# Kernel optimization log

Measured on AMD Instinct MI355X. Metric: run time of the kernel, lower is better.

Reference implementation:

```python
import jax, jax.numpy as jnp
import numpy as np

SIZE_MIN, SIZE_MAX = 10.0, 40.0
CROP = 28


def convert_to_box_list(x):
    # [B, C, W, H] -> [W*H, B, C]
    b, c, w, h = x.shape
    return jnp.transpose(x, (2, 3, 0, 1)).reshape(w * h, b, c)


def invert_convert_to_box_list(x, w, h):
    # [W*H, B, C] -> [B, C, W, H]
    n, b, c = x.shape
    return jnp.transpose(x.reshape(w, h, b, c), (2, 3, 0, 1))


def bilinear_sample(img, x, y):
    # img: [C, W, H]; x, y: pixel coords of shape S -> [C, *S]; zero outside.
    C, W, H = img.shape
    x0 = jnp.floor(x); y0 = jnp.floor(y)
    x1 = x0 + 1.0; y1 = y0 + 1.0
    wx1 = x - x0; wx0 = 1.0 - wx1
    wy1 = y - y0; wy0 = 1.0 - wy1
    def fetch(xi, yi):
        valid = ((xi >= 0) & (xi < W) & (yi >= 0) & (yi < H)).astype(img.dtype)
        xc = jnp.clip(xi, 0, W - 1).astype(jnp.int32)
        yc = jnp.clip(yi, 0, H - 1).astype(jnp.int32)
        return img[:, xc, yc] * valid
    return (fetch(x0, y0) * (wx0 * wy0) + fetch(x1, y0) * (wx1 * wy0)
            + fetch(x0, y1) * (wx0 * wy1) + fetch(x1, y1) * (wx1 * wy1))


def crop(bx, by, bw, bh, big, ws, hs):
    # bx..bh: [k, B]; big: [B, C, W, H] -> [k, B, C, ws, hs]
    u = (jnp.arange(ws) + 0.5) / ws
    v = (jnp.arange(hs) + 0.5) / hs
    xs = bx[..., None] - 0.5 * bw[..., None] + u * bw[..., None] - 0.5  # [k,B,ws]
    ys = by[..., None] - 0.5 * bh[..., None] + v * bh[..., None] - 0.5  # [k,B,hs]
    def one(xr, yr, img):
        X = jnp.broadcast_to(xr[:, None], (ws, hs))
        Y = jnp.broadcast_to(yr[None, :], (ws, hs))
        return bilinear_sample(img, X, Y)
    return jax.vmap(jax.vmap(one, (0, 0, 0)), (0, 0, None))(xs, ys, big)


def uncrop(bx, by, bw, bh, small, Wb, Hb):
    # small: [k, B, C, ws, hs] -> [k, B, C, Wb, Hb] (zero outside each box)
    ws, hs = small.shape[-2], small.shape[-1]
    Xc = jnp.arange(Wb) + 0.5
    Yc = jnp.arange(Hb) + 0.5
    xs = (Xc - (bx[..., None] - 0.5 * bw[..., None])) / bw[..., None] * ws - 0.5
    ys = (Yc - (by[..., None] - 0.5 * bh[..., None])) / bh[..., None] * hs - 0.5
    def one(xr, yr, img):
        X = jnp.broadcast_to(xr[:, None], (Wb, Hb))
        Y = jnp.broadcast_to(yr[None, :], (Wb, Hb))
        return bilinear_sample(img, X, Y)
    return jax.vmap(jax.vmap(one, (0, 0, 0)), (0, 0, 0))(xs, ys, small)


def tmaps_to_bb(tmaps, W_raw, H_raw):
    # tmaps: [B, 4, nw, nh] in (0,1) -> box lists [n_all, B]
    nw, nh = tmaps.shape[-2], tmaps.shape[-1]
    tx, ty, tw, th = tmaps[:, 0], tmaps[:, 1], tmaps[:, 2], tmaps[:, 3]
    ix = jnp.arange(nw, dtype=tmaps.dtype)[:, None]
    iy = jnp.arange(nh, dtype=tmaps.dtype)[None, :]
    bx_map = W_raw * (ix + tx) / nw
    by_map = H_raw * (iy + ty) / nh
    bw_map = SIZE_MIN + (SIZE_MAX - SIZE_MIN) * tw
    bh_map = SIZE_MIN + (SIZE_MAX - SIZE_MIN) * th
    tolist = lambda m: convert_to_box_list(m[:, None]).squeeze(-1)
    return tolist(bx_map), tolist(by_map), tolist(bw_map), tolist(bh_map)


def forward_core(logit_mu, zwhere_mu, zwhere_std, eps_zwhere, eps_zinstance,
                 features, w_zwhere, b_zwhere, w_enc, b_enc, w_dec, b_dec, n_objects_max):
    B, Cf, W_raw, H_raw = features.shape
    nw, nh = logit_mu.shape[-2], logit_mu.shape[-1]

    # zwhere posterior sample + KL vs N(0,1)
    zwhere_sample_map = zwhere_mu + zwhere_std * eps_zwhere
    zwhere_kl_map = 0.5 * (zwhere_mu ** 2 + zwhere_std ** 2) - jnp.log(zwhere_std) - 0.5

    # decode zwhere (1x1 conv) -> sigmoid tmaps -> boxes
    tmaps = jax.nn.sigmoid(jnp.einsum('bzwh,cz->bcwh', zwhere_sample_map, w_zwhere)
                           + b_zwhere[None, :, None, None])
    bx_all, by_all, bw_all, bh_all = tmaps_to_bb(tmaps, W_raw, H_raw)

    area_all = bw_all * bh_all
    area_map = invert_convert_to_box_list(area_all[..., None], nw, nh)

    # c sample = logit map (deterministic relaxation of the DPP/Bernoulli sample)
    c_sample_map = logit_mu
    prob_map = jax.nn.sigmoid(c_sample_map)
    c_all = convert_to_box_list(c_sample_map).squeeze(-1)   # [n_all, B]
    prob_all = convert_to_box_list(prob_map).squeeze(-1)

    # top-k per batch element (indices constant wrt grads)
    k = min(n_objects_max, c_all.shape[0])
    idx = jax.lax.stop_gradient(jax.lax.top_k(c_all.T, k)[1].T)  # [k, B]
    take = lambda t: jnp.take_along_axis(t, idx, axis=0)
    c_few, prob_few = take(c_all), take(prob_all)
    bx_few, by_few, bw_few, bh_few = take(bx_all), take(by_all), take(bw_all), take(bh_all)

    zwhere_sample_all = convert_to_box_list(zwhere_sample_map)  # [n_all, B, Z]
    zwhere_kl_all = convert_to_box_list(zwhere_kl_map)
    idx_z = idx[..., None]
    zwhere_sample_few = jnp.take_along_axis(zwhere_sample_all, idx_z, axis=0)
    zwhere_kl_few = jnp.take_along_axis(zwhere_kl_all, idx_z, axis=0)

    # crop full-res features at the k boxes -> [k, B, Cf, CROP, CROP]
    cropped = crop(bx_few, by_few, bw_few, bh_few, features, CROP, CROP)

    # encoder zinstance (flatten + linear -> mu, std)
    flat = cropped.reshape(k, B, -1)
    enc = jnp.einsum('kbf,df->kbd', flat, w_enc) + b_enc
    dim_z = enc.shape[-1] // 2
    zi_mu = enc[..., :dim_z]
    zi_std = jax.nn.softplus(enc[..., dim_z:]) + 1e-4
    zi_sample = zi_mu + zi_std * eps_zinstance
    zi_kl = 0.5 * (zi_mu ** 2 + zi_std ** 2) - jnp.log(zi_std) - 0.5

    # decoder zinstance (linear -> [k, B, 2, CROP, CROP])
    dec = jnp.einsum('kbz,fz->kbf', zi_sample, w_dec) + b_dec
    raw = dec.reshape(k, B, 2, CROP, CROP)
    small = jnp.concatenate([jax.nn.softplus(raw[..., :1, :, :]),
                             jax.nn.sigmoid(raw[..., 1:, :, :])], axis=-3)

    big_stuff = uncrop(bx_few, by_few, bw_few, bh_few,
                       small * c_few[..., None, None, None], W_raw, H_raw)
    big_weight = big_stuff[..., :1, :, :]
    big_img = big_stuff[..., 1:, :, :]

    # from_weights_to_masks over box dim (dim=-5 of [k,B,1,W,H])
    sum_w = jnp.sum(big_weight, axis=0, keepdims=True)
    big_mask = jnp.tanh(sum_w) * (big_weight / jnp.maximum(sum_w, 1e-6))
    big_mask_non = jnp.tanh(big_weight)

    return (prob_map, area_map, c_few, prob_few, bx_few, by_few, bw_few, bh_few,
            big_mask, big_mask_non, big_img,
            zwhere_sample_few, zwhere_kl_few, zi_sample, zi_kl)


def setup_inputs() -> dict:
    key = jax.random.key(0)
    ks = jax.random.split(key, 9)
    B, NW, NH = 8, 32, 32
    W_RAW = H_RAW = 128
    CF, ZW, ZI, K = 32, 8, 32, 48
    fan_in = CF * CROP * CROP
    return {
        "logit_mu": jax.random.normal(ks[0], (B, 1, NW, NH), jnp.float32),
        "zwhere_mu": 0.5 * jax.random.normal(ks[1], (B, ZW, NW, NH), jnp.float32),
        "zwhere_std": jax.random.uniform(ks[2], (B, ZW, NW, NH), jnp.float32, 0.1, 1.0),
        "eps_zwhere": jax.random.normal(ks[3], (B, ZW, NW, NH), jnp.float32),
        "eps_zinstance": jax.random.normal(ks[4], (K, B, ZI), jnp.float32),
        "features": jax.random.normal(ks[5], (B, CF, W_RAW, H_RAW), jnp.float32),
        "w_zwhere": 0.3 * jax.random.normal(ks[6], (4, ZW), jnp.float32),
        "b_zwhere": jnp.zeros((4,), jnp.float32),
        "w_enc": jax.random.normal(ks[7], (2 * ZI, fan_in), jnp.float32) / np.sqrt(fan_in).astype(np.float32),
        "b_enc": jnp.zeros((2 * ZI,), jnp.float32),
        "w_dec": jax.random.normal(ks[8], (2 * CROP * CROP, ZI), jnp.float32) / np.sqrt(ZI).astype(np.float32),
        "b_dec": jnp.zeros((2 * CROP * CROP,), jnp.float32),
        "n_objects_max": 48,
    }


def reference(logit_mu, zwhere_mu, zwhere_std, eps_zwhere, eps_zinstance, features,
              w_zwhere, b_zwhere, w_enc, b_enc, w_dec, b_dec, n_objects_max):
    return forward_core(logit_mu, zwhere_mu, zwhere_std, eps_zwhere, eps_zinstance,
                        features, w_zwhere, b_zwhere, w_enc, b_enc, w_dec, b_dec,
                        n_objects_max)
```

## Files before the change

### kernel.cpp

```cpp
#include <hip/hip_runtime.h>
#include <math.h>

#define B 8
#define NWD 32
#define NHD 32
#define NBOX 1024
#define ZWD 8
#define ZID 32
#define KOBJ 48
#define CFEAT 32
#define WRAW 128
#define HRAW 128
#define CR 28
#define CR2 784
#define FAN 25088
#define KB 384

#define OFF_PROB   0
#define OFF_AREA   8192
#define OFF_CFEW   16384
#define OFF_PFEW   16768
#define OFF_BXF    17152
#define OFF_BYF    17536
#define OFF_BWF    17920
#define OFF_BHF    18304
#define OFF_BMASK  18688
#define OFF_BMASKN 6310144
#define OFF_BIMG   12601600
#define OFF_ZWS    18893056
#define OFF_ZWK    18896128
#define OFF_ZIS    18899200
#define OFF_ZIK    18911488

#define WS_SMALL 32768

#define SCR_PART 0
#define SCR_WBF  2752512

#define FSPLIT 112
#define FPB 224
#define MKB 16
#define KSTR 232

typedef __attribute__((ext_vector_type(8))) short bfrag;
typedef __attribute__((ext_vector_type(4))) float f32x4;

__device__ __forceinline__ float sigm(float x){ return 1.0f/(1.0f+expf(-x)); }
__device__ __forceinline__ float softpl(float x){ return fmaxf(x,0.0f) + log1pf(expf(-fabsf(x))); }
__device__ __forceinline__ float ftanh(float x){
  float t = __expf(2.0f*x);
  return 1.0f - __fdividef(2.0f, t + 1.0f);
}
__device__ __forceinline__ unsigned short f2bf(float f){
  unsigned u = __float_as_uint(f);
  unsigned r = u + 0x7FFFu + ((u >> 16) & 1u);
  return (unsigned short)(r >> 16);
}
__device__ __forceinline__ unsigned okey(float f){
  unsigned b = __float_as_uint(f);
  return b ^ ((b & 0x80000000u) ? 0xFFFFFFFFu : 0x80000000u);
}

__global__ __launch_bounds__(256) void wconv_kernel(
    const float* __restrict__ wenc, unsigned short* __restrict__ wbf){
  const size_t i0 = ((size_t)blockIdx.x*256 + threadIdx.x)*8;
  float4 a = *(const float4*)&wenc[i0];
  float4 b = *(const float4*)&wenc[i0+4];
  unsigned long long p0 = (unsigned long long)f2bf(a.x)
    | ((unsigned long long)f2bf(a.y) << 16)
    | ((unsigned long long)f2bf(a.z) << 32)
    | ((unsigned long long)f2bf(a.w) << 48);
  unsigned long long p1 = (unsigned long long)f2bf(b.x)
    | ((unsigned long long)f2bf(b.y) << 16)
    | ((unsigned long long)f2bf(b.z) << 32)
    | ((unsigned long long)f2bf(b.w) << 48);
  *(unsigned long long*)&wbf[i0]   = p0;
  *(unsigned long long*)&wbf[i0+4] = p1;
}

__global__ __launch_bounds__(256) void maps_topk_kernel(
    const float* __restrict__ logit, const float* __restrict__ zmu,
    const float* __restrict__ zstd, const float* __restrict__ zeps,
    const float* __restrict__ wz, const float* __restrict__ bz,
    float* __restrict__ out){
  const int b  = blockIdx.x >> 2;
  const int sb = blockIdx.x & 3;
  const int tid = threadIdx.x;
  __shared__ __align__(16) unsigned su[NBOX];
  #pragma unroll
  for (int u = 0; u < 4; u++){
    int j = tid + u*256;
    su[j] = okey(logit[b*NBOX + j]);
  }
  const int n = sb*256 + tid;
  const int w = n >> 5, h = n & 31;
  float acc0=bz[0], acc1=bz[1], acc2=bz[2], acc3=bz[3];
  #pragma unroll
  for(int z=0; z<ZWD; z++){
    int id = ((b*ZWD + z)*NWD + w)*NHD + h;
    float s = zmu[id] + zstd[id]*zeps[id];
    acc0 += s*wz[0*ZWD+z]; acc1 += s*wz[1*ZWD+z];
    acc2 += s*wz[2*ZWD+z]; acc3 += s*wz[3*ZWD+z];
  }
  float tx=sigm(acc0), ty=sigm(acc1), tw=sigm(acc2), th=sigm(acc3);
  float bx = (128.0f*((float)w + tx))/32.0f;
  float by = (128.0f*((float)h + ty))/32.0f;
  float bwv = 10.0f + 30.0f*tw;
  float bhv = 10.0f + 30.0f*th;
  float lg = logit[b*NBOX + n];
  out[OFF_PROB + b*NBOX + n] = sigm(lg);
  out[OFF_AREA + b*NBOX + n] = bwv*bhv;
  __syncthreads();
  const unsigned ui = su[n];
  const uint4* su4 = (const uint4*)su;
  int rank = 0;
  #pragma unroll 4
  for (int jq = 0; jq < NBOX/4; jq++){
    uint4 v = su4[jq];
    int j = jq*4;
    rank += (v.x > ui || (v.x == ui && j   < n)) ? 1 : 0;
    rank += (v.y > ui || (v.y == ui && j+1 < n)) ? 1 : 0;
    rank += (v.z > ui || (v.z == ui && j+2 < n)) ? 1 : 0;
    rank += (v.w > ui || (v.w == ui && j+3 < n)) ? 1 : 0;
  }
  if (rank < KOBJ){
    out[OFF_CFEW + rank*B + b] = lg;
    out[OFF_PFEW + rank*B + b] = sigm(lg);
    out[OFF_BXF  + rank*B + b] = bx;
    out[OFF_BYF  + rank*B + b] = by;
    out[OFF_BWF  + rank*B + b] = bwv;
    out[OFF_BHF  + rank*B + b] = bhv;
    #pragma unroll
    for(int z=0; z<ZWD; z++){
      int id = ((b*ZWD + z)*NWD + w)*NHD + h;
      float mu = zmu[id], sd = zstd[id];
      out[OFF_ZWS + (rank*B+b)*ZWD + z] = mu + sd*zeps[id];
      out[OFF_ZWK + (rank*B+b)*ZWD + z] = 0.5f*(mu*mu + sd*sd) - logf(sd) - 0.5f;
    }
  }
}

__global__ __launch_bounds__(256, 4) void enc_kernel(
    const float* __restrict__ feat, const unsigned short* __restrict__ wbf,
    const float* __restrict__ outc, float* __restrict__ part){
  __shared__ __align__(16) unsigned short wl[64*KSTR];
  __shared__ __align__(16) unsigned short cl[MKB*KSTR];
  __shared__ float rAx[MKB], rSx[MKB], rAy[MKB], rSy[MKB];
  const int tid = threadIdx.x;
  const int fs  = blockIdx.x % FSPLIT;
  const int kb0 = (blockIdx.x / FSPLIT) * MKB;
  if (tid < MKB){
    float bx = outc[OFF_BXF + kb0 + tid];
    float by = outc[OFF_BYF + kb0 + tid];
    float bw = outc[OFF_BWF + kb0 + tid];
    float bh = outc[OFF_BHF + kb0 + tid];
    float sx = bw * (1.0f/(float)CR), sy = bh * (1.0f/(float)CR);
    rSx[tid] = sx; rSy[tid] = sy;
    rAx[tid] = bx - 0.5f*bw + 0.5f*sx - 0.5f;
    rAy[tid] = by - 0.5f*bh + 0.5f*sy - 0.5f;
  }
  __syncthreads();
  const int fc0 = fs*FPB;
  #pragma unroll
  for (int u = 0; u < 7; u++){
    int idx = u*256 + tid;
    int dd = idx / 28, q = idx - dd*28;
    bfrag w8 = *(const bfrag*)&wbf[(size_t)dd*FAN + fc0 + q*8];
    *(bfrag*)&wl[dd*KSTR + q*8] = w8;
  }
  #pragma unroll 2
  for (int u = 0; u < 14; u++){
    int idx = u*256 + tid;
    int rr = idx / FPB, ff = idx - rr*FPB;
    int f = fc0 + ff;
    int c = f / CR2; int p = f - c*CR2;
    int i = p / CR;  int j = p - i*CR;
    int kb = kb0 + rr;
    const float* img = feat + (size_t)((kb & (B-1))*CFEAT + c)*(WRAW*HRAW);
    float x = fmaf((float)i, rSx[rr], rAx[rr]);
    float y = fmaf((float)j, rSy[rr], rAy[rr]);
    float x0f = floorf(x), y0f = floorf(y);
    int x0 = (int)x0f, y0 = (int)y0f;
    float wx1 = x - x0f, wx0 = 1.0f - wx1;
    float wy1 = y - y0f, wy0 = 1.0f - wy1;
    if ((unsigned)x0     >= WRAW) wx0 = 0.f;
    if ((unsigned)(x0+1) >= WRAW) wx1 = 0.f;
    if ((unsigned)y0     >= HRAW) wy0 = 0.f;
    if ((unsigned)(y0+1) >= HRAW) wy1 = 0.f;
    int x0c = min(max(x0,0),WRAW-1), x1c = min(max(x0+1,0),WRAW-1);
    int y0c = min(max(y0,0),HRAW-1), y1c = min(max(y0+1,0),HRAW-1);
    const float* r0p = img + x0c*HRAW;
    const float* r1p = img + x1c*HRAW;
    float v = (r0p[y0c]*wy0 + r0p[y1c]*wy1)*wx0
            + (r1p[y0c]*wy0 + r1p[y1c]*wy1)*wx1;
    cl[rr*KSTR + ff] = f2bf(v);
  }
  __syncthreads();
  const int lane = tid & 63, wv = tid >> 6;
  const int lr = lane & 15, lg = lane >> 4;
  f32x4 acc = {0.f,0.f,0.f,0.f};
  const unsigned short* arow = &cl[lr*KSTR + lg*8];
  const unsigned short* brow = &wl[(wv*16 + lr)*KSTR + lg*8];
  #pragma unroll
  for (int s = 0; s < 7; s++){
    bfrag a = *(const bfrag*)(arow + s*32);
    bfrag b = *(const bfrag*)(brow + s*32);
    acc = __builtin_amdgcn_mfma_f32_16x16x32_bf16(a, b, acc, 0, 0, 0);
  }
  float* dst = part + ((size_t)fs*KB + kb0)*64;
  #pragma unroll
  for (int r = 0; r < 4; r++){
    int row = lg*4 + r;
    dst[row*64 + wv*16 + lr] = acc[r];
  }
}

__global__ __launch_bounds__(256) void zi_dec_kernel(
    const float* __restrict__ part, const float* __restrict__ benc,
    const float* __restrict__ ieps, const float* __restrict__ wdec,
    const float* __restrict__ bdec, float* __restrict__ out,
    float* __restrict__ ws){
  int kb = blockIdx.x;
  int d = threadIdx.x & 63, seg = threadIdx.x >> 6;
  float s0=0.f, s1=0.f, s2=0.f, s3=0.f;
  for (int f = seg; f < FSPLIT; f += 16){
    s0 += part[((size_t)(f   )*KB + kb)*64 + d];
    s1 += part[((size_t)(f+ 4)*KB + kb)*64 + d];
    s2 += part[((size_t)(f+ 8)*KB + kb)*64 + d];
    s3 += part[((size_t)(f+12)*KB + kb)*64 + d];
  }
  __shared__ float red[4][64];
  __shared__ float zs[ZID];
  __shared__ float cf_s;
  red[seg][d] = (s0+s1) + (s2+s3);
  __syncthreads();
  if (threadIdx.x < ZID){
    int dd = threadIdx.x;
    float mu = benc[dd]     + red[0][dd]     + red[1][dd]     + red[2][dd]     + red[3][dd];
    float pe = benc[ZID+dd] + red[0][ZID+dd] + red[1][ZID+dd] + red[2][ZID+dd] + red[3][ZID+dd];
    float sd = softpl(pe) + 1e-4f;
    float zsv = mu + sd*ieps[kb*ZID + dd];
    out[OFF_ZIS + kb*ZID + dd] = zsv;
    out[OFF_ZIK + kb*ZID + dd] = 0.5f*(mu*mu + sd*sd) - logf(sd) - 0.5f;
    zs[dd] = zsv;
  }
  if (threadIdx.x == 0) cf_s = out[OFF_CFEW + kb];
  __syncthreads();
  float cf = cf_s;
  for (int f = threadIdx.x; f < 2*CR2; f += 256){
    float a = bdec[f];
    #pragma unroll
    for (int q = 0; q < 8; q++){
      float4 w4 = *(const float4*)&wdec[f*ZID + q*4];
      a = fmaf(zs[q*4+0], w4.x, a);
      a = fmaf(zs[q*4+1], w4.y, a);
      a = fmaf(zs[q*4+2], w4.z, a);
      a = fmaf(zs[q*4+3], w4.w, a);
    }
    float v = (f < CR2) ? softpl(a) : sigm(a);
    ws[WS_SMALL + (size_t)kb*(2*CR2) + f] = v*cf;
  }
}

__global__ __launch_bounds__(256) void uncrop_compose_kernel(
    const float* __restrict__ ws, float* __restrict__ out){
  const int t = blockIdx.x*256 + threadIdx.x;
  const int b = t >> 14, p = t & 16383;
  const int X = p >> 7, Y = p & 127;
  __shared__ float sAx[KOBJ], sSx[KOBJ], sAy[KOBJ], sSy[KOBJ];
  if (threadIdx.x < KOBJ){
    int k = threadIdx.x;
    float bx = out[OFF_BXF + k*B + b], bw = out[OFF_BWF + k*B + b];
    float by = out[OFF_BYF + k*B + b], bh = out[OFF_BHF + k*B + b];
    float ix = __fdividef((float)CR, bw), iy = __fdividef((float)CR, bh);
    sSx[k] = ix; sAx[k] = (0.5f*bw - bx)*ix - 0.5f;
    sSy[k] = iy; sAy[k] = (0.5f*bh - by)*iy - 0.5f;
  }
  __syncthreads();
  const float xc = (float)X + 0.5f, yc = (float)Y + 0.5f;
  float wr[KOBJ];
  float sum = 0.f;
  #pragma unroll
  for (int k = 0; k < KOBJ; k++){
    float x = fmaf(xc, sSx[k], sAx[k]);
    float y = fmaf(yc, sSy[k], sAy[k]);
    const float* sm = ws + WS_SMALL + (size_t)(k*B + b)*(2*CR2);
    float x0f = floorf(x), y0f = floorf(y);
    int x0 = (int)x0f, y0 = (int)y0f;
    float wx1 = x - x0f, wx0 = 1.0f - wx1;
    float wy1 = y - y0f, wy0 = 1.0f - wy1;
    if ((unsigned)x0     >= CR) wx0 = 0.f;
    if ((unsigned)(x0+1) >= CR) wx1 = 0.f;
    if ((unsigned)y0     >= CR) wy0 = 0.f;
    if ((unsigned)(y0+1) >= CR) wy1 = 0.f;
    int x0c = min(max(x0,0),CR-1), x1c = min(max(x0+1,0),CR-1);
    int y0c = min(max(y0,0),CR-1), y1c = min(max(y0+1,0),CR-1);
    const float* r0 = sm + x0c*CR;
    const float* r1 = sm + x1c*CR;
    float v0 = (r0[y0c]*wy0 + r0[y1c]*wy1)*wx0 + (r1[y0c]*wy0 + r1[y1c]*wy1)*wx1;
    const float* q0 = r0 + CR2;
    const float* q1 = r1 + CR2;
    float v1 = (q0[y0c]*wy0 + q0[y1c]*wy1)*wx0 + (q1[y0c]*wy0 + q1[y1c]*wy1)*wx1;
    wr[k] = v0; sum += v0;
    out[OFF_BIMG + (size_t)(k*B + b)*16384 + p] = v1;
  }
  float th = ftanh(sum);
  float inv = 1.0f / fmaxf(sum, 1e-6f);
  #pragma unroll
  for (int k = 0; k < KOBJ; k++){
    size_t o = (size_t)(k*B + b)*16384 + p;
    out[OFF_BMASK  + o] = th * (wr[k] * inv);
    out[OFF_BMASKN + o] = ftanh(wr[k]);
  }
}

extern "C" void kernel_launch(void* const* d_in, const int* in_sizes, int n_in,
                              void* d_out, int out_size, void* d_ws, size_t ws_size,
                              hipStream_t stream) {
  (void)in_sizes; (void)n_in; (void)out_size; (void)ws_size;
  const float* logit = (const float*)d_in[0];
  const float* zmu   = (const float*)d_in[1];
  const float* zstd  = (const float*)d_in[2];
  const float* zeps  = (const float*)d_in[3];
  const float* ieps  = (const float*)d_in[4];
  const float* feat  = (const float*)d_in[5];
  const float* wz    = (const float*)d_in[6];
  const float* bz    = (const float*)d_in[7];
  const float* wenc  = (const float*)d_in[8];
  const float* benc  = (const float*)d_in[9];
  const float* wdec  = (const float*)d_in[10];
  const float* bdec  = (const float*)d_in[11];
  float* out = (float*)d_out;
  float* ws  = (float*)d_ws;
  float* scr = out + OFF_BMASK;
  float* part = scr + SCR_PART;
  unsigned short* wbf = (unsigned short*)(scr + SCR_WBF);

  wconv_kernel        <<<(FAN*64)/(256*8), 256, 0, stream>>>(wenc, wbf);
  maps_topk_kernel    <<<B*4, 256, 0, stream>>>(logit, zmu, zstd, zeps, wz, bz, out);
  enc_kernel          <<<(KB/MKB)*FSPLIT, 256, 0, stream>>>(feat, wbf, out, part);
  zi_dec_kernel       <<<KB, 256, 0, stream>>>(part, benc, ieps, wdec, bdec, out, ws);
  uncrop_compose_kernel<<<(B*WRAW*HRAW)/256, 256, 0, stream>>>(ws, out);
}
```

Baseline: 100.9 us.

## Pre-swizzle encoder weights into MFMA fragment order and precompute bilinear taps

The weight conversion kernel now writes bf16 weights already permuted into per-lane MFMA B-fragment order. The encoder therefore loads B fragments straight from global memory instead of staging a 64x224 weight tile through shared memory. Per-row and per-column bilinear offsets and weights are computed once per block into shared-memory tables rather than for every sampled element. Dropping the weight tile cuts LDS use, and launch bounds are raised to allow 8 blocks per CU for more occupancy. The tradeoff is that the MFMA loop now waits on global-memory latency for its B operands.

```diff
diff --git a/kernel.cpp b/kernel.cpp
--- a/kernel.cpp
+++ b/kernel.cpp
@@ -35,12 +35,13 @@
 #define WS_SMALL 32768
 
 #define SCR_PART 0
-#define SCR_WBF  2752512
+#define SCR_WT   2752512
 
 #define FSPLIT 112
 #define FPB 224
 #define MKB 16
 #define KSTR 232
+#define TAPN (MKB*28)
 
 typedef __attribute__((ext_vector_type(8))) short bfrag;
 typedef __attribute__((ext_vector_type(4))) float f32x4;
@@ -62,10 +63,19 @@
 }
 
 __global__ __launch_bounds__(256) void wconv_kernel(
-    const float* __restrict__ wenc, unsigned short* __restrict__ wbf){
-  const size_t i0 = ((size_t)blockIdx.x*256 + threadIdx.x)*8;
-  float4 a = *(const float4*)&wenc[i0];
-  float4 b = *(const float4*)&wenc[i0+4];
+    const float* __restrict__ wenc, unsigned short* __restrict__ wt){
+  const int gid = blockIdx.x*256 + threadIdx.x;
+  const int lane = gid & 63;
+  const int rest = gid >> 6;
+  const int t = rest & 3;
+  const int rest2 = rest >> 2;
+  const int s = rest2 % 7;
+  const int fs = rest2 / 7;
+  const int d = t*16 + (lane & 15);
+  const int k0 = fs*FPB + s*32 + (lane >> 4)*8;
+  const float* src = wenc + (size_t)d*FAN + k0;
+  float4 a = *(const float4*)src;
+  float4 b = *(const float4*)(src + 4);
   unsigned long long p0 = (unsigned long long)f2bf(a.x)
     | ((unsigned long long)f2bf(a.y) << 16)
     | ((unsigned long long)f2bf(a.z) << 32)
@@ -74,8 +84,9 @@
     | ((unsigned long long)f2bf(b.y) << 16)
     | ((unsigned long long)f2bf(b.z) << 32)
     | ((unsigned long long)f2bf(b.w) << 48);
-  *(unsigned long long*)&wbf[i0]   = p0;
-  *(unsigned long long*)&wbf[i0+4] = p1;
+  unsigned short* dst = wt + (size_t)gid*8;
+  *(unsigned long long*)dst       = p0;
+  *(unsigned long long*)(dst + 4) = p1;
 }
 
 __global__ __launch_bounds__(256) void maps_topk_kernel(
@@ -140,11 +151,12 @@
   }
 }
 
-__global__ __launch_bounds__(256, 4) void enc_kernel(
-    const float* __restrict__ feat, const unsigned short* __restrict__ wbf,
+__global__ __launch_bounds__(256, 8) void enc_kernel(
+    const float* __restrict__ feat, const unsigned short* __restrict__ wt,
     const float* __restrict__ outc, float* __restrict__ part){
-  __shared__ __align__(16) unsigned short wl[64*KSTR];
   __shared__ __align__(16) unsigned short cl[MKB*KSTR];
+  __shared__ float2 wxs[TAPN]; __shared__ int2 xos[TAPN];
+  __shared__ float2 wys[TAPN]; __shared__ int2 yos[TAPN];
   __shared__ float rAx[MKB], rSx[MKB], rAy[MKB], rSy[MKB];
   const int tid = threadIdx.x;
   const int fs  = blockIdx.x % FSPLIT;
@@ -160,14 +172,27 @@
     rAy[tid] = by - 0.5f*bh + 0.5f*sy - 0.5f;
   }
   __syncthreads();
+  #pragma unroll
+  for (int it = 0; it < 4; it++){
+    int idx = it*256 + tid;
+    if (idx < 2*TAPN){
+      int isy = idx >= TAPN;
+      int q = idx - (isy ? TAPN : 0);
+      int rr = q / 28, i = q - rr*28;
+      float A = isy ? rAy[rr] : rAx[rr];
+      float S = isy ? rSy[rr] : rSx[rr];
+      float x = fmaf((float)i, S, A);
+      float x0f = floorf(x); int x0 = (int)x0f;
+      float w1 = x - x0f, w0 = 1.0f - w1;
+      if ((unsigned)x0     >= WRAW) w0 = 0.f;
+      if ((unsigned)(x0+1) >= WRAW) w1 = 0.f;
+      int c0 = min(max(x0,0),WRAW-1), c1 = min(max(x0+1,0),WRAW-1);
+      if (isy){ wys[q] = make_float2(w0,w1); yos[q] = make_int2(c0, c1); }
+      else    { wxs[q] = make_float2(w0,w1); xos[q] = make_int2(c0*HRAW, c1*HRAW); }
+    }
+  }
+  __syncthreads();
   const int fc0 = fs*FPB;
-  #pragma unroll
-  for (int u = 0; u < 7; u++){
-    int idx = u*256 + tid;
-    int dd = idx / 28, q = idx - dd*28;
-    bfrag w8 = *(const bfrag*)&wbf[(size_t)dd*FAN + fc0 + q*8];
-    *(bfrag*)&wl[dd*KSTR + q*8] = w8;
-  }
   #pragma unroll 2
   for (int u = 0; u < 14; u++){
     int idx = u*256 + tid;
@@ -175,36 +200,23 @@
     int f = fc0 + ff;
     int c = f / CR2; int p = f - c*CR2;
     int i = p / CR;  int j = p - i*CR;
-    int kb = kb0 + rr;
-    const float* img = feat + (size_t)((kb & (B-1))*CFEAT + c)*(WRAW*HRAW);
-    float x = fmaf((float)i, rSx[rr], rAx[rr]);
-    float y = fmaf((float)j, rSy[rr], rAy[rr]);
-    float x0f = floorf(x), y0f = floorf(y);
-    int x0 = (int)x0f, y0 = (int)y0f;
-    float wx1 = x - x0f, wx0 = 1.0f - wx1;
-    float wy1 = y - y0f, wy0 = 1.0f - wy1;
-    if ((unsigned)x0     >= WRAW) wx0 = 0.f;
-    if ((unsigned)(x0+1) >= WRAW) wx1 = 0.f;
-    if ((unsigned)y0     >= HRAW) wy0 = 0.f;
-    if ((unsigned)(y0+1) >= HRAW) wy1 = 0.f;
-    int x0c = min(max(x0,0),WRAW-1), x1c = min(max(x0+1,0),WRAW-1);
-    int y0c = min(max(y0,0),HRAW-1), y1c = min(max(y0+1,0),HRAW-1);
-    const float* r0p = img + x0c*HRAW;
-    const float* r1p = img + x1c*HRAW;
-    float v = (r0p[y0c]*wy0 + r0p[y1c]*wy1)*wx0
-            + (r1p[y0c]*wy0 + r1p[y1c]*wy1)*wx1;
+    const float* img = feat + (size_t)(((kb0+rr) & (B-1))*CFEAT + c)*(WRAW*HRAW);
+    float2 wx = wxs[rr*28 + i]; int2 xo = xos[rr*28 + i];
+    float2 wy = wys[rr*28 + j]; int2 yo = yos[rr*28 + j];
+    float v = (img[xo.x+yo.x]*wy.x + img[xo.x+yo.y]*wy.y)*wx.x
+            + (img[xo.y+yo.x]*wy.x + img[xo.y+yo.y]*wy.y)*wx.y;
     cl[rr*KSTR + ff] = f2bf(v);
   }
   __syncthreads();
   const int lane = tid & 63, wv = tid >> 6;
   const int lr = lane & 15, lg = lane >> 4;
   f32x4 acc = {0.f,0.f,0.f,0.f};
-  const unsigned short* arow = &cl[lr*KSTR + lg*8];
-  const unsigned short* brow = &wl[(wv*16 + lr)*KSTR + lg*8];
+  const unsigned short* arow  = &cl[lr*KSTR + lg*8];
+  const unsigned short* bbase = wt + (size_t)fs*14336 + wv*512 + lane*8;
   #pragma unroll
   for (int s = 0; s < 7; s++){
     bfrag a = *(const bfrag*)(arow + s*32);
-    bfrag b = *(const bfrag*)(brow + s*32);
+    bfrag b = *(const bfrag*)(bbase + s*2048);
     acc = __builtin_amdgcn_mfma_f32_16x16x32_bf16(a, b, acc, 0, 0, 0);
   }
   float* dst = part + ((size_t)fs*KB + kb0)*64;
@@ -334,11 +346,11 @@
   float* ws  = (float*)d_ws;
   float* scr = out + OFF_BMASK;
   float* part = scr + SCR_PART;
-  unsigned short* wbf = (unsigned short*)(scr + SCR_WBF);
-
-  wconv_kernel        <<<(FAN*64)/(256*8), 256, 0, stream>>>(wenc, wbf);
+  unsigned short* wt = (unsigned short*)(scr + SCR_WT);
+
+  wconv_kernel        <<<(FAN*64)/(256*8), 256, 0, stream>>>(wenc, wt);
   maps_topk_kernel    <<<B*4, 256, 0, stream>>>(logit, zmu, zstd, zeps, wz, bz, out);
-  enc_kernel          <<<(KB/MKB)*FSPLIT, 256, 0, stream>>>(feat, wbf, out, part);
+  enc_kernel          <<<(KB/MKB)*FSPLIT, 256, 0, stream>>>(feat, wt, out, part);
   zi_dec_kernel       <<<KB, 256, 0, stream>>>(part, benc, ieps, wdec, bdec, out, ws);
   uncrop_compose_kernel<<<(B*WRAW*HRAW)/256, 256, 0, stream>>>(ws, out);
 }
```

Measured after the change: 95.50 us. -5.3%, faster.
